# Performance work log

Measured on AMD Instinct MI355X. Metric: run time of the kernel, lower is better.

The kernel has to match this reference:

```python
import jax, jax.numpy as jnp
import numpy as np

NUM_CLASSES = 1000  # label vocabulary size (matches fill_max for label)
B = 16384
D_IN = 1024   # image_embedding
D_OUT = 256   # projection_dim


def setup_inputs() -> dict:
    key = jax.random.key(0)
    k = jax.random.split(key, 6)
    x = jax.random.normal(k[0], (B, D_IN), dtype=jnp.float32)
    label = jax.random.randint(k[1], (B,), 0, NUM_CLASSES, dtype=jnp.int64)
    scale = 1.0 / np.sqrt(D_IN)
    W1_w = jax.random.normal(k[2], (D_OUT, D_IN), dtype=jnp.float32) * scale
    W1_b = jax.random.normal(k[3], (D_OUT,), dtype=jnp.float32) * scale
    W2_w = jax.random.normal(k[4], (D_OUT, D_IN), dtype=jnp.float32) * scale
    W2_b = jax.random.normal(k[5], (D_OUT,), dtype=jnp.float32) * scale
    return {"x": x, "label": label, "W1_w": W1_w, "W1_b": W1_b,
            "W2_w": W2_w, "W2_b": W2_b}


def reference(x, label, W1_w, W1_b, W2_w, W2_b):
    # Leave-one-group-out mean, vectorized via segment sums.
    # Original: for each i, mean of x[label != label_i] (detached); zeros if none.
    b = x.shape[0]
    xd = jax.lax.stop_gradient(x)  # .detach() in the torch code
    label_sum = jax.ops.segment_sum(xd, label, num_segments=NUM_CLASSES)          # [C, D_IN]
    label_cnt = jax.ops.segment_sum(jnp.ones((b,), dtype=x.dtype), label,
                                    num_segments=NUM_CLASSES)                     # [C]
    total_sum = xd.sum(axis=0)                                                    # [D_IN]
    other_sum = total_sum[None, :] - label_sum[label]                             # [B, D_IN]
    other_cnt = jnp.asarray(b, x.dtype) - label_cnt[label]                        # [B]
    calculate_mean = jnp.where(other_cnt[:, None] > 0,
                               other_sum / jnp.maximum(other_cnt, 1)[:, None],
                               jnp.zeros((), x.dtype))                            # [B, D_IN]
    # W1(x) + W2(calculate_mean)  (torch Linear: y = x @ W.T + b)
    return x @ W1_w.T + W1_b + calculate_mean @ W2_w.T + W2_b
```

## Files before the change

### kernel.cpp

```cpp
#include <hip/hip_runtime.h>
#include <hip/hip_bf16.h>

constexpr int B      = 16384;
constexpr int D_IN   = 1024;
constexpr int D_OUT  = 256;
constexpr int NCLS   = 1000;
constexpr int CPAD   = 1024;

constexpr size_t OFF_XB   = 0;
constexpr size_t OFF_WB   = OFF_XB  + (size_t)B * D_IN * 2;
constexpr size_t OFF_S    = OFF_WB  + (size_t)512 * D_IN * 2;
constexpr size_t OFF_Z    = OFF_S   + (size_t)CPAD * D_IN * 4;
constexpr size_t OFF_T    = OFF_Z   + (size_t)CPAD * D_OUT * 4;
constexpr size_t OFF_CNT  = OFF_T   + (size_t)D_IN * 4;
constexpr size_t OFF_OFFS = OFF_CNT + (size_t)CPAD * 4;
constexpr size_t OFF_CUR  = OFF_OFFS+ (size_t)CPAD * 4;
constexpr size_t OFF_ROWL = OFF_CUR + (size_t)CPAD * 4;

typedef short bf16x8 __attribute__((ext_vector_type(8)));
typedef float f32x4  __attribute__((ext_vector_type(4)));

__device__ __forceinline__ unsigned short f2bf(float f) {
    unsigned int u = __float_as_uint(f);
    return (unsigned short)((u + 0x7FFFu + ((u >> 16) & 1u)) >> 16);
}

__device__ __forceinline__ void cvt8(const float4& a, const float4& b, unsigned short* dst) {
    union { unsigned short u[8]; bf16x8 v; } r;
    r.u[0] = f2bf(a.x); r.u[1] = f2bf(a.y); r.u[2] = f2bf(a.z); r.u[3] = f2bf(a.w);
    r.u[4] = f2bf(b.x); r.u[5] = f2bf(b.y); r.u[6] = f2bf(b.z); r.u[7] = f2bf(b.w);
    *(bf16x8*)dst = r.v;
}

__device__ __forceinline__ ushort4 f2bf4(const float4& a) {
    ushort4 r;
    r.x = f2bf(a.x); r.y = f2bf(a.y); r.z = f2bf(a.z); r.w = f2bf(a.w);
    return r;
}

__device__ __forceinline__ void async16(const unsigned short* g, unsigned short* l) {
    __builtin_amdgcn_global_load_lds(
        (const __attribute__((address_space(1))) void*)g,
        (__attribute__((address_space(3))) void*)l,
        16, 0, 0);
}

__global__ void cvtw_zero_kernel(const float* __restrict__ W1, const float* __restrict__ W2,
                                 unsigned short* __restrict__ Wb,
                                 int* __restrict__ cnt, float* __restrict__ T,
                                 float* __restrict__ Z) {
    int lin = blockIdx.x * blockDim.x + threadIdx.x;
    int i = lin * 8;
    const float* src = (i < D_OUT * D_IN) ? (W1 + i) : (W2 + (i - D_OUT * D_IN));
    float4 a = *(const float4*)(src);
    float4 b = *(const float4*)(src + 4);
    cvt8(a, b, Wb + i);
    if (lin < CPAD) { cnt[lin] = 0; T[lin] = 0.f; }
    *(float4*)(Z + (size_t)lin * 4) = float4{0.f, 0.f, 0.f, 0.f};
}

__global__ void hist_kernel(const int* __restrict__ label, int* __restrict__ cnt) {
    int i = blockIdx.x * blockDim.x + threadIdx.x;
    atomicAdd(&cnt[label[i]], 1);
}

__global__ __launch_bounds__(1024)
void scan_kernel(const int* __restrict__ cnt, int* __restrict__ offs, int* __restrict__ cursor) {
    __shared__ int bufA[1024];
    __shared__ int bufB[1024];
    int t = threadIdx.x;
    int v = cnt[t];
    bufA[t] = v;
    __syncthreads();
    int* src = bufA;
    int* dst = bufB;
    for (int off = 1; off < 1024; off <<= 1) {
        int sv = src[t];
        if (t >= off) sv += src[t - off];
        dst[t] = sv;
        __syncthreads();
        int* tmp = src; src = dst; dst = tmp;
    }
    int excl = src[t] - v;
    offs[t] = excl;
    cursor[t] = excl;
}

__global__ void scatter_kernel(const int* __restrict__ label,
                               int* __restrict__ cursor,
                               int* __restrict__ rowlist) {
    int i = blockIdx.x * blockDim.x + threadIdx.x;
    int c = label[i];
    int p = atomicAdd(&cursor[c], 1);
    rowlist[p] = i;
}

__global__ void segsum_kernel(const float* __restrict__ x,
                              const int* __restrict__ offs,
                              const int* __restrict__ cnt,
                              const int* __restrict__ rowlist,
                              float* __restrict__ s,
                              unsigned short* __restrict__ xb) {
    int c = blockIdx.x;
    int col = threadIdx.x * 4;
    float4 acc = {0.f, 0.f, 0.f, 0.f};
    if (c < NCLS) {
        int o = offs[c], n = cnt[c];
        int r = 0;
        for (; r + 4 <= n; r += 4) {
            int i0 = rowlist[o + r + 0];
            int i1 = rowlist[o + r + 1];
            int i2 = rowlist[o + r + 2];
            int i3 = rowlist[o + r + 3];
            float4 v0 = *(const float4*)(x + (size_t)i0 * D_IN + col);
            float4 v1 = *(const float4*)(x + (size_t)i1 * D_IN + col);
            float4 v2 = *(const float4*)(x + (size_t)i2 * D_IN + col);
            float4 v3 = *(const float4*)(x + (size_t)i3 * D_IN + col);
            *(ushort4*)(xb + (size_t)i0 * D_IN + col) = f2bf4(v0);
            *(ushort4*)(xb + (size_t)i1 * D_IN + col) = f2bf4(v1);
            *(ushort4*)(xb + (size_t)i2 * D_IN + col) = f2bf4(v2);
            *(ushort4*)(xb + (size_t)i3 * D_IN + col) = f2bf4(v3);
            acc.x += (v0.x + v1.x) + (v2.x + v3.x);
            acc.y += (v0.y + v1.y) + (v2.y + v3.y);
            acc.z += (v0.z + v1.z) + (v2.z + v3.z);
            acc.w += (v0.w + v1.w) + (v2.w + v3.w);
        }
        for (; r < n; ++r) {
            int i0 = rowlist[o + r];
            float4 v = *(const float4*)(x + (size_t)i0 * D_IN + col);
            *(ushort4*)(xb + (size_t)i0 * D_IN + col) = f2bf4(v);
            acc.x += v.x; acc.y += v.y; acc.z += v.z; acc.w += v.w;
        }
    }
    *(float4*)(s + (size_t)c * D_IN + col) = acc;
}

__global__ void tsum_kernel(const float* __restrict__ s, float* __restrict__ T) {
    int col = threadIdx.x * 4;
    int c0 = blockIdx.x * 16;
    float4 acc = {0.f, 0.f, 0.f, 0.f};
#pragma unroll 4
    for (int c = 0; c < 16; ++c) {
        float4 v = *(const float4*)(s + (size_t)(c0 + c) * D_IN + col);
        acc.x += v.x; acc.y += v.y; acc.z += v.z; acc.w += v.w;
    }
    atomicAdd(&T[col + 0], acc.x);
    atomicAdd(&T[col + 1], acc.y);
    atomicAdd(&T[col + 2], acc.z);
    atomicAdd(&T[col + 3], acc.w);
}

__global__ __launch_bounds__(256)
void meanz_kernel(const float* __restrict__ s,
                  const float* __restrict__ T,
                  const int* __restrict__ cnt,
                  const unsigned short* __restrict__ Wb,
                  const float* __restrict__ b2,
                  float* __restrict__ Z) {
    __shared__ unsigned short As[64 * 32];
    __shared__ unsigned short Bs[64 * 32];

    const int tid  = threadIdx.x;
    const int wave = tid >> 6;
    const int lane = tid & 63;
    const int quad = lane >> 4;
    const int l16  = lane & 15;
    const int bm   = blockIdx.x * 64;
    const int bn   = blockIdx.y * 64;
    const int kb   = blockIdx.z * 256;
    const int wm   = (wave >> 1) * 32;
    const int wn   = (wave & 1) * 32;

    const int arow = tid >> 2;
    const int akc  = (tid & 3) * 8;

    const int cls = bm + arow;
    const int d   = B - cnt[cls];
    const float scale = (d > 0) ? 1.f / (float)d : 0.f;
    const float* sp = s + (size_t)cls * D_IN + akc;
    const float* tp = T + akc;

    const int bidx = wave * 64 + lane;
    const int brow = bidx >> 2;
    const int bkc  = (bidx & 3) * 8;
    const unsigned short* bp = Wb + (size_t)(256 + bn + brow) * D_IN + bkc;

    f32x4 acc[2][2] = {};

    for (int k0 = kb; k0 < kb + 256; k0 += 32) {
        float4 s0 = *(const float4*)(sp + k0);
        float4 s1 = *(const float4*)(sp + k0 + 4);
        float4 t0 = *(const float4*)(tp + k0);
        float4 t1 = *(const float4*)(tp + k0 + 4);
        __syncthreads();
        async16(bp + k0, Bs + wave * 512);
        float4 m0 = {(t0.x - s0.x) * scale, (t0.y - s0.y) * scale,
                     (t0.z - s0.z) * scale, (t0.w - s0.w) * scale};
        float4 m1 = {(t1.x - s1.x) * scale, (t1.y - s1.y) * scale,
                     (t1.z - s1.z) * scale, (t1.w - s1.w) * scale};
        cvt8(m0, m1, As + arow * 32 + akc);
        __syncthreads();

        bf16x8 af[2], bfr[2];
#pragma unroll
        for (int t = 0; t < 2; ++t) {
            af[t]  = *(const bf16x8*)&As[(wm + t * 16 + l16) * 32 + quad * 8];
            bfr[t] = *(const bf16x8*)&Bs[(wn + t * 16 + l16) * 32 + quad * 8];
        }
#pragma unroll
        for (int i = 0; i < 2; ++i)
#pragma unroll
            for (int j = 0; j < 2; ++j)
                acc[i][j] = __builtin_amdgcn_mfma_f32_16x16x32_bf16(af[i], bfr[j], acc[i][j], 0, 0, 0);
    }

    const bool addb = (blockIdx.z == 0);
#pragma unroll
    for (int j = 0; j < 2; ++j) {
        const int n = bn + wn + j * 16 + l16;
        const float bias = addb ? b2[n] : 0.f;
#pragma unroll
        for (int i = 0; i < 2; ++i)
#pragma unroll
            for (int r = 0; r < 4; ++r) {
                const int c = bm + wm + i * 16 + quad * 4 + r;
                atomicAdd(&Z[(size_t)c * D_OUT + n], acc[i][j][r] + bias);
            }
    }
}

__global__ __launch_bounds__(256)
void gemm1_kernel(const unsigned short* __restrict__ xb,
                  const unsigned short* __restrict__ Wb,
                  const float* __restrict__ b1,
                  const float* __restrict__ Z,
                  const int* __restrict__ label,
                  float* __restrict__ out) {
    __shared__ unsigned short As[64 * 32];
    __shared__ unsigned short Bs[64 * 32];

    const int tid  = threadIdx.x;
    const int wave = tid >> 6;
    const int lane = tid & 63;
    const int quad = lane >> 4;
    const int l16  = lane & 15;
    const int bm   = blockIdx.x * 64;
    const int bn   = blockIdx.y * 64;
    const int wm   = (wave >> 1) * 32;
    const int wn   = (wave & 1) * 32;

    const int idx = wave * 64 + lane;
    const int row = idx >> 2;
    const int kc  = (idx & 3) * 8;
    const unsigned short* ap = xb + (size_t)(bm + row) * D_IN + kc;
    const unsigned short* bp = Wb + (size_t)(bn + row) * D_IN + kc;

    f32x4 acc[2][2] = {};

    for (int k0 = 0; k0 < D_IN; k0 += 32) {
        __syncthreads();
        async16(ap + k0, As + wave * 512);
        async16(bp + k0, Bs + wave * 512);
        __syncthreads();

        bf16x8 af[2], bfr[2];
#pragma unroll
        for (int t = 0; t < 2; ++t) {
            af[t]  = *(const bf16x8*)&As[(wm + t * 16 + l16) * 32 + quad * 8];
            bfr[t] = *(const bf16x8*)&Bs[(wn + t * 16 + l16) * 32 + quad * 8];
        }
#pragma unroll
        for (int i = 0; i < 2; ++i)
#pragma unroll
            for (int j = 0; j < 2; ++j)
                acc[i][j] = __builtin_amdgcn_mfma_f32_16x16x32_bf16(af[i], bfr[j], acc[i][j], 0, 0, 0);
    }

    int zrow[2][4];
#pragma unroll
    for (int i = 0; i < 2; ++i)
#pragma unroll
        for (int r = 0; r < 4; ++r)
            zrow[i][r] = label[bm + wm + i * 16 + quad * 4 + r] * D_OUT;

#pragma unroll
    for (int j = 0; j < 2; ++j) {
        const int n = bn + wn + j * 16 + l16;
        const float bias = b1[n];
#pragma unroll
        for (int i = 0; i < 2; ++i)
#pragma unroll
            for (int r = 0; r < 4; ++r) {
                const int m = bm + wm + i * 16 + quad * 4 + r;
                out[(size_t)m * D_OUT + n] = acc[i][j][r] + bias + Z[zrow[i][r] + n];
            }
    }
}

extern "C" void kernel_launch(void* const* d_in, const int* in_sizes, int n_in,
                              void* d_out, int out_size, void* d_ws, size_t ws_size,
                              hipStream_t stream) {
    const float* x    = (const float*)d_in[0];
    const int*   lab  = (const int*)d_in[1];
    const float* W1_w = (const float*)d_in[2];
    const float* W1_b = (const float*)d_in[3];
    const float* W2_w = (const float*)d_in[4];
    const float* W2_b = (const float*)d_in[5];
    float* out = (float*)d_out;

    char* ws = (char*)d_ws;
    unsigned short* xb = (unsigned short*)(ws + OFF_XB);
    unsigned short* Wb = (unsigned short*)(ws + OFF_WB);
    float* s   = (float*)(ws + OFF_S);
    float* Z   = (float*)(ws + OFF_Z);
    float* T   = (float*)(ws + OFF_T);
    int* cnt     = (int*)(ws + OFF_CNT);
    int* offs    = (int*)(ws + OFF_OFFS);
    int* cursor  = (int*)(ws + OFF_CUR);
    int* rowlist = (int*)(ws + OFF_ROWL);

    cvtw_zero_kernel<<<256, 256, 0, stream>>>(W1_w, W2_w, Wb, cnt, T, Z);
    hist_kernel<<<64, 256, 0, stream>>>(lab, cnt);
    scan_kernel<<<1, 1024, 0, stream>>>(cnt, offs, cursor);
    scatter_kernel<<<64, 256, 0, stream>>>(lab, cursor, rowlist);
    segsum_kernel<<<CPAD, 256, 0, stream>>>(x, offs, cnt, rowlist, s, xb);
    tsum_kernel<<<64, 256, 0, stream>>>(s, T);
    dim3 zgrid(CPAD / 64, D_OUT / 64, 4);
    meanz_kernel<<<zgrid, 256, 0, stream>>>(s, T, cnt, Wb, W2_b, Z);
    dim3 ggrid(B / 64, D_OUT / 64);
    gemm1_kernel<<<ggrid, 256, 0, stream>>>(xb, Wb, W1_b, Z, lab, out);
}
```

Before: 164.6 us.

## Fuse prep kernels into one launch, fold total-sum into segsum, enlarge GEMM tile

```diff
diff --git a/kernel.cpp b/kernel.cpp
--- a/kernel.cpp
+++ b/kernel.cpp
@@ -45,35 +45,41 @@
         16, 0, 0);
 }
 
-__global__ void cvtw_zero_kernel(const float* __restrict__ W1, const float* __restrict__ W2,
-                                 unsigned short* __restrict__ Wb,
-                                 int* __restrict__ cnt, float* __restrict__ T,
-                                 float* __restrict__ Z) {
-    int lin = blockIdx.x * blockDim.x + threadIdx.x;
-    int i = lin * 8;
-    const float* src = (i < D_OUT * D_IN) ? (W1 + i) : (W2 + (i - D_OUT * D_IN));
-    float4 a = *(const float4*)(src);
-    float4 b = *(const float4*)(src + 4);
-    cvt8(a, b, Wb + i);
-    if (lin < CPAD) { cnt[lin] = 0; T[lin] = 0.f; }
-    *(float4*)(Z + (size_t)lin * 4) = float4{0.f, 0.f, 0.f, 0.f};
-}
-
-__global__ void hist_kernel(const int* __restrict__ label, int* __restrict__ cnt) {
-    int i = blockIdx.x * blockDim.x + threadIdx.x;
-    atomicAdd(&cnt[label[i]], 1);
-}
-
 __global__ __launch_bounds__(1024)
-void scan_kernel(const int* __restrict__ cnt, int* __restrict__ offs, int* __restrict__ cursor) {
-    __shared__ int bufA[1024];
-    __shared__ int bufB[1024];
+void prep_kernel(const float* __restrict__ W1, const float* __restrict__ W2,
+                 unsigned short* __restrict__ Wb,
+                 float* __restrict__ T, float* __restrict__ Z,
+                 const int* __restrict__ label,
+                 int* __restrict__ cnt, int* __restrict__ offs,
+                 int* __restrict__ rowlist) {
+    __shared__ int hA[1024];
+    __shared__ int hB[1024];
+
+    if (blockIdx.x < 64) {
+        int lin = blockIdx.x * 1024 + threadIdx.x;
+        int i = lin * 8;
+        const float* src = (i < D_OUT * D_IN) ? (W1 + i) : (W2 + (i - D_OUT * D_IN));
+        float4 a = *(const float4*)(src);
+        float4 b = *(const float4*)(src + 4);
+        cvt8(a, b, Wb + i);
+        if (lin < D_IN) T[lin] = 0.f;
+        *(float4*)(Z + (size_t)lin * 4) = float4{0.f, 0.f, 0.f, 0.f};
+        return;
+    }
+
     int t = threadIdx.x;
-    int v = cnt[t];
-    bufA[t] = v;
+    hA[t] = 0;
     __syncthreads();
-    int* src = bufA;
-    int* dst = bufB;
+    int lab[16];
+#pragma unroll
+    for (int r = 0; r < 16; ++r) {
+        lab[r] = label[t + r * 1024];
+        atomicAdd(&hA[lab[r]], 1);
+    }
+    __syncthreads();
+    int v = hA[t];
+    int* src = hA;
+    int* dst = hB;
     for (int off = 1; off < 1024; off <<= 1) {
         int sv = src[t];
         if (t >= off) sv += src[t - off];
@@ -82,17 +88,15 @@
         int* tmp = src; src = dst; dst = tmp;
     }
     int excl = src[t] - v;
+    cnt[t]  = v;
     offs[t] = excl;
-    cursor[t] = excl;
-}
-
-__global__ void scatter_kernel(const int* __restrict__ label,
-                               int* __restrict__ cursor,
-                               int* __restrict__ rowlist) {
-    int i = blockIdx.x * blockDim.x + threadIdx.x;
-    int c = label[i];
-    int p = atomicAdd(&cursor[c], 1);
-    rowlist[p] = i;
+    dst[t]  = excl;
+    __syncthreads();
+#pragma unroll
+    for (int r = 0; r < 16; ++r) {
+        int p = atomicAdd(&dst[lab[r]], 1);
+        rowlist[p] = t + r * 1024;
+    }
 }
 
 __global__ void segsum_kernel(const float* __restrict__ x,
@@ -100,7 +104,8 @@
                               const int* __restrict__ cnt,
                               const int* __restrict__ rowlist,
                               float* __restrict__ s,
-                              unsigned short* __restrict__ xb) {
+                              unsigned short* __restrict__ xb,
+                              float* __restrict__ T) {
     int c = blockIdx.x;
     int col = threadIdx.x * 4;
     float4 acc = {0.f, 0.f, 0.f, 0.f};
@@ -133,21 +138,12 @@
         }
     }
     *(float4*)(s + (size_t)c * D_IN + col) = acc;
-}
-
-__global__ void tsum_kernel(const float* __restrict__ s, float* __restrict__ T) {
-    int col = threadIdx.x * 4;
-    int c0 = blockIdx.x * 16;
-    float4 acc = {0.f, 0.f, 0.f, 0.f};
-#pragma unroll 4
-    for (int c = 0; c < 16; ++c) {
-        float4 v = *(const float4*)(s + (size_t)(c0 + c) * D_IN + col);
-        acc.x += v.x; acc.y += v.y; acc.z += v.z; acc.w += v.w;
-    }
-    atomicAdd(&T[col + 0], acc.x);
-    atomicAdd(&T[col + 1], acc.y);
-    atomicAdd(&T[col + 2], acc.z);
-    atomicAdd(&T[col + 3], acc.w);
+    if (c < NCLS) {
+        atomicAdd(&T[col + 0], acc.x);
+        atomicAdd(&T[col + 1], acc.y);
+        atomicAdd(&T[col + 2], acc.z);
+        atomicAdd(&T[col + 3], acc.w);
+    }
 }
 
 __global__ __launch_bounds__(256)
@@ -236,49 +232,66 @@
                   const float* __restrict__ Z,
                   const int* __restrict__ label,
                   float* __restrict__ out) {
-    __shared__ unsigned short As[64 * 32];
-    __shared__ unsigned short Bs[64 * 32];
+    __shared__ unsigned short As[2][128][32];
+    __shared__ unsigned short Bs[2][64][32];
 
     const int tid  = threadIdx.x;
     const int wave = tid >> 6;
     const int lane = tid & 63;
     const int quad = lane >> 4;
     const int l16  = lane & 15;
-    const int bm   = blockIdx.x * 64;
+    const int bm   = blockIdx.x * 128;
     const int bn   = blockIdx.y * 64;
-    const int wm   = (wave >> 1) * 32;
+    const int wm   = (wave >> 1) * 64;
     const int wn   = (wave & 1) * 32;
 
-    const int idx = wave * 64 + lane;
-    const int row = idx >> 2;
-    const int kc  = (idx & 3) * 8;
-    const unsigned short* ap = xb + (size_t)(bm + row) * D_IN + kc;
-    const unsigned short* bp = Wb + (size_t)(bn + row) * D_IN + kc;
-
-    f32x4 acc[2][2] = {};
-
-    for (int k0 = 0; k0 < D_IN; k0 += 32) {
-        __syncthreads();
-        async16(ap + k0, As + wave * 512);
-        async16(bp + k0, Bs + wave * 512);
-        __syncthreads();
-
-        bf16x8 af[2], bfr[2];
-#pragma unroll
-        for (int t = 0; t < 2; ++t) {
-            af[t]  = *(const bf16x8*)&As[(wm + t * 16 + l16) * 32 + quad * 8];
-            bfr[t] = *(const bf16x8*)&Bs[(wn + t * 16 + l16) * 32 + quad * 8];
+    const unsigned short* aps[4];
+#pragma unroll
+    for (int rr = 0; rr < 4; ++rr) {
+        int dd = rr * 256 + tid;
+        int h = dd >> 9, r = (dd >> 2) & 127, c = dd & 3;
+        aps[rr] = xb + (size_t)(bm + r) * D_IN + h * 32 + c * 8;
+    }
+    const unsigned short* bps[2];
+#pragma unroll
+    for (int rr = 0; rr < 2; ++rr) {
+        int dd = rr * 256 + tid;
+        int h = dd >> 8, r = (dd >> 2) & 63, c = dd & 3;
+        bps[rr] = Wb + (size_t)(bn + r) * D_IN + h * 32 + c * 8;
+    }
+
+    f32x4 acc[4][2] = {};
+
+    for (int k0 = 0; k0 < D_IN; k0 += 64) {
+        __syncthreads();
+#pragma unroll
+        for (int rr = 0; rr < 4; ++rr)
+            async16(aps[rr] + k0, &As[0][0][0] + rr * 2048 + wave * 512);
+#pragma unroll
+        for (int rr = 0; rr < 2; ++rr)
+            async16(bps[rr] + k0, &Bs[0][0][0] + rr * 2048 + wave * 512);
+        __syncthreads();
+
+#pragma unroll
+        for (int ks = 0; ks < 2; ++ks) {
+            bf16x8 af[4], bfr[2];
+#pragma unroll
+            for (int i = 0; i < 4; ++i)
+                af[i] = *(const bf16x8*)&As[ks][wm + i * 16 + l16][quad * 8];
+#pragma unroll
+            for (int j = 0; j < 2; ++j)
+                bfr[j] = *(const bf16x8*)&Bs[ks][wn + j * 16 + l16][quad * 8];
+#pragma unroll
+            for (int i = 0; i < 4; ++i)
+#pragma unroll
+                for (int j = 0; j < 2; ++j)
+                    acc[i][j] = __builtin_amdgcn_mfma_f32_16x16x32_bf16(af[i], bfr[j], acc[i][j], 0, 0, 0);
         }
-#pragma unroll
-        for (int i = 0; i < 2; ++i)
-#pragma unroll
-            for (int j = 0; j < 2; ++j)
-                acc[i][j] = __builtin_amdgcn_mfma_f32_16x16x32_bf16(af[i], bfr[j], acc[i][j], 0, 0, 0);
-    }
-
-    int zrow[2][4];
-#pragma unroll
-    for (int i = 0; i < 2; ++i)
+    }
+
+    int zrow[4][4];
+#pragma unroll
+    for (int i = 0; i < 4; ++i)
 #pragma unroll
         for (int r = 0; r < 4; ++r)
             zrow[i][r] = label[bm + wm + i * 16 + quad * 4 + r] * D_OUT;
@@ -288,7 +301,7 @@
         const int n = bn + wn + j * 16 + l16;
         const float bias = b1[n];
 #pragma unroll
-        for (int i = 0; i < 2; ++i)
+        for (int i = 0; i < 4; ++i)
 #pragma unroll
             for (int r = 0; r < 4; ++r) {
                 const int m = bm + wm + i * 16 + quad * 4 + r;
@@ -316,17 +329,12 @@
     float* T   = (float*)(ws + OFF_T);
     int* cnt     = (int*)(ws + OFF_CNT);
     int* offs    = (int*)(ws + OFF_OFFS);
-    int* cursor  = (int*)(ws + OFF_CUR);
     int* rowlist = (int*)(ws + OFF_ROWL);
 
-    cvtw_zero_kernel<<<256, 256, 0, stream>>>(W1_w, W2_w, Wb, cnt, T, Z);
-    hist_kernel<<<64, 256, 0, stream>>>(lab, cnt);
-    scan_kernel<<<1, 1024, 0, stream>>>(cnt, offs, cursor);
-    scatter_kernel<<<64, 256, 0, stream>>>(lab, cursor, rowlist);
-    segsum_kernel<<<CPAD, 256, 0, stream>>>(x, offs, cnt, rowlist, s, xb);
-    tsum_kernel<<<64, 256, 0, stream>>>(s, T);
+    prep_kernel<<<65, 1024, 0, stream>>>(W1_w, W2_w, Wb, T, Z, lab, cnt, offs, rowlist);
+    segsum_kernel<<<CPAD, 256, 0, stream>>>(x, offs, cnt, rowlist, s, xb, T);
     dim3 zgrid(CPAD / 64, D_OUT / 64, 4);
     meanz_kernel<<<zgrid, 256, 0, stream>>>(s, T, cnt, Wb, W2_b, Z);
-    dim3 ggrid(B / 64, D_OUT / 64);
+    dim3 ggrid(B / 128, D_OUT / 64);
     gemm1_kernel<<<ggrid, 256, 0, stream>>>(xb, Wb, W1_b, Z, lab, out);
 }
```

After: 238.9 us. +45.1%, slower.
